# Optimization experiments

Hardware: AMD Instinct MI355X
Metric: run time of the kernel (lower is better)

Reference implementation:

```python
import jax, jax.numpy as jnp
import numpy as np

B = 131072
K = 1024
D = 16 * 8  # hard-coded feature dim in the torch module


def setup_inputs() -> dict:
    key = jax.random.key(0)
    kx, kw = jax.random.split(key)
    x = jax.random.normal(kx, (B, D), dtype=jnp.float32)
    # xavier_normal_ init: std = sqrt(2 / (fan_in + fan_out)) = sqrt(2 / (K + D))
    std = np.sqrt(2.0 / (K + D)).astype(np.float32)
    cluster_weights = jax.random.normal(kw, (K, D), dtype=jnp.float32) * std
    return {"x": x, "cluster_weights": cluster_weights}


def reference(x, cluster_weights):
    bn = x.shape[0]
    k = cluster_weights.shape[0]
    x = x.reshape(bn, -1)  # [B, D]
    # (same math as the original broadcasted (x - w)^2 sum, without the [B,K,D] blow-up)
    x2 = jnp.sum(x * x, axis=1, keepdims=True)               # [B, 1]
    w2 = jnp.sum(cluster_weights * cluster_weights, axis=1)  # [K]
    d = x2 + w2[None, :] - 2.0 * jnp.matmul(x, cluster_weights.T)  # [B, K]
    cl = jnp.argmin(d, axis=1)  # [B] int
    # distance to assigned centroid, summed
    inertia_loss = jnp.sum(jnp.take_along_axis(d, cl[:, None], axis=1))
    # xe_loss = sum_{i,j} (1 if i==j else -1) * <w_i, w_j>
    #         = 2 * trace(W W^T) - sum(W W^T)
    G = jnp.matmul(cluster_weights, cluster_weights.T)  # [K, K]
    xe_loss = 2.0 * jnp.trace(G) - jnp.sum(G)
    return inertia_loss / bn, xe_loss / k, cl
```

## Files before the change

kernel.cpp:

```cpp
#include <hip/hip_runtime.h>
#include <float.h>
#include <limits.h>
#include <math.h>


#define TAU 1e-3f

using bf16x8 = __attribute__((ext_vector_type(8))) short;
using f32x4  = __attribute__((ext_vector_type(4))) float;
using s16x4  = __attribute__((ext_vector_type(4))) short;

static __device__ __forceinline__ short f2bf_trunc(float f) {
    return (short)(__float_as_uint(f) >> 16);
}
static __device__ __forceinline__ float bf2f(short h) {
    return __uint_as_float(((unsigned int)(unsigned short)h) << 16);
}
static __device__ __forceinline__ bool lexlt(float v1, int i1, float v2, int i2) {
    return v1 < v2 || (v1 == v2 && i1 < i2);
}
static __device__ __forceinline__ void gload_lds16(const void* g, void* l) {
    __builtin_amdgcn_global_load_lds(
        (const __attribute__((address_space(1))) unsigned int*)g,
        (__attribute__((address_space(3))) unsigned int*)l, 16, 0, 0);
}
#define FENCE() do { asm volatile("" ::: "memory"); __builtin_amdgcn_sched_barrier(0); } while (0)

__global__ void wprep_kernel(const float* __restrict__ W, float* __restrict__ w2,
                             short* __restrict__ whl, int write_whl)
{
    const int k = blockIdx.x;
    const int d = threadIdx.x;
    float v = W[(size_t)k * 128 + d];
    float sq = v * v;
    for (int off = 1; off < 64; off <<= 1) sq += __shfl_xor(sq, off, 64);
    __shared__ float p[2];
    if ((d & 63) == 0) p[d >> 6] = sq;
    __syncthreads();
    if (d == 0) w2[k] = p[0] + p[1];
    if (write_whl) {
        short h = f2bf_trunc(v);
        short l = f2bf_trunc(v - bf2f(h));
        const int tile = k >> 6, c = k & 63;
        size_t base = (size_t)tile * 16384 + (size_t)(c >> 4) * 2048 + (size_t)(d >> 5) * 512
                    + (size_t)((d >> 3) & 3) * 128 + (size_t)(c & 15) * 8 + (size_t)(d & 7);
        whl[base]        = h;
        whl[base + 8192] = l;
    }
}

__global__ __launch_bounds__(512, 4)
void dist_argmin_mfma(const float* __restrict__ X, const short* __restrict__ whl,
                      const float* __restrict__ w2g, float* __restrict__ cl_out,
                      double* __restrict__ inertia_acc,
                      int* __restrict__ flag_cnt, int* __restrict__ flag_rows,
                      int flag_cap)
{
    __shared__ __align__(16) char smem[72320];
    char*   lB0  = smem;
    char*   lB1  = smem + 32768;
    float*  lw2  = (float*)(smem + 65536);
    float*  lx2  = (float*)(smem + 69632);
    int*    mscr = (int*)(smem + 70144);
    double* dred = (double*)(smem + 72192);

    const int tid    = threadIdx.x;
    const int lane   = tid & 63;
    const int laneLo = lane & 15;
    const int laneHi = lane >> 4;
    const int wid    = tid >> 6;
    const int rowg   = wid >> 1;
    const int colg   = wid & 1;
    const int rowbase = blockIdx.x * 128;

    lw2[tid]       = w2g[tid];
    lw2[tid + 512] = w2g[tid + 512];

    bf16x8 ah[2][4], al[2][4];
    #pragma unroll
    for (int m = 0; m < 2; ++m) {
        const float* xp = X + (size_t)(rowbase + rowg * 32 + m * 16 + laneLo) * 128 + laneHi * 8;
        float s = 0.f;
        #pragma unroll
        for (int k0b = 0; k0b < 4; ++k0b) {
            float4 v0 = *reinterpret_cast<const float4*>(xp + k0b * 32);
            float4 v1 = *reinterpret_cast<const float4*>(xp + k0b * 32 + 4);
            float fv[8] = {v0.x, v0.y, v0.z, v0.w, v1.x, v1.y, v1.z, v1.w};
            bf16x8 hv, lv;
            #pragma unroll
            for (int u = 0; u < 8; ++u) {
                s = fmaf(fv[u], fv[u], s);
                short h = f2bf_trunc(fv[u]);
                short l = f2bf_trunc(fv[u] - bf2f(h));
                hv[u] = h; lv[u] = l;
            }
            ah[m][k0b] = hv; al[m][k0b] = lv;
        }
        s += __shfl_xor(s, 16, 64);
        s += __shfl_xor(s, 32, 64);
        if (colg == 0 && laneHi == 0) lx2[rowg * 32 + m * 16 + laneLo] = s;
    }
    asm volatile("s_waitcnt lgkmcnt(0)" ::: "memory");
    __builtin_amdgcn_sched_barrier(0);

    const char* wsrc = (const char*)whl;
    #pragma unroll
    for (int q = 0; q < 4; ++q)
        gload_lds16(wsrc + wid * 4096 + q * 1024 + lane * 16,
                    lB0 + wid * 4096 + q * 1024);
    wsrc += 32768;

    float t1v[2][4], t2v[2][4];
    int   t1i[2][4];
    #pragma unroll
    for (int m = 0; m < 2; ++m)
        #pragma unroll
        for (int r = 0; r < 4; ++r) {
            t1v[m][r] = FLT_MAX; t2v[m][r] = FLT_MAX; t1i[m][r] = INT_MAX;
        }

    const float* w2p = lw2 + colg * 32 + laneLo;
    int colbase = colg * 32 + laneLo;

    auto compute = [&](const char* pB) {
        const char* pBb = pB + colg * 8192 + lane * 16;
        __builtin_amdgcn_s_setprio(1);
        #pragma unroll
        for (int nt = 0; nt < 2; ++nt) {
            float w2v = w2p[nt * 16];
            f32x4 a0 = (f32x4){0.f, 0.f, 0.f, 0.f};
            f32x4 a1 = (f32x4){0.f, 0.f, 0.f, 0.f};
            #pragma unroll
            for (int k0b = 0; k0b < 4; ++k0b) {
                bf16x8 bh = *reinterpret_cast<const bf16x8*>(pBb + nt * 4096 + k0b * 1024);
                bf16x8 bl = *reinterpret_cast<const bf16x8*>(pBb + 16384 + nt * 4096 + k0b * 1024);
                a0 = __builtin_amdgcn_mfma_f32_16x16x32_bf16(ah[0][k0b], bh, a0, 0, 0, 0);
                a0 = __builtin_amdgcn_mfma_f32_16x16x32_bf16(ah[0][k0b], bl, a0, 0, 0, 0);
                a0 = __builtin_amdgcn_mfma_f32_16x16x32_bf16(al[0][k0b], bh, a0, 0, 0, 0);
                a1 = __builtin_amdgcn_mfma_f32_16x16x32_bf16(ah[1][k0b], bh, a1, 0, 0, 0);
                a1 = __builtin_amdgcn_mfma_f32_16x16x32_bf16(ah[1][k0b], bl, a1, 0, 0, 0);
                a1 = __builtin_amdgcn_mfma_f32_16x16x32_bf16(al[1][k0b], bh, a1, 0, 0, 0);
            }
            const int col = colbase + nt * 16;
            #pragma unroll
            for (int r = 0; r < 4; ++r) {
                float dv0 = fmaf(-2.f, a0[r], w2v);
                t2v[0][r] = fminf(t2v[0][r], fmaxf(t1v[0][r], dv0));
                t1i[0][r] = (dv0 < t1v[0][r]) ? col : t1i[0][r];
                t1v[0][r] = fminf(t1v[0][r], dv0);
                float dv1 = fmaf(-2.f, a1[r], w2v);
                t2v[1][r] = fminf(t2v[1][r], fmaxf(t1v[1][r], dv1));
                t1i[1][r] = (dv1 < t1v[1][r]) ? col : t1i[1][r];
                t1v[1][r] = fminf(t1v[1][r], dv1);
            }
        }
        __builtin_amdgcn_s_setprio(0);
    };

    const char* cur = lB0;
    char*       nxt = lB1;
    #pragma unroll 1
    for (int t = 0; t < 15; ++t) {
        #pragma unroll
        for (int q = 0; q < 4; ++q)
            gload_lds16(wsrc + wid * 4096 + q * 1024 + lane * 16,
                        nxt + wid * 4096 + q * 1024);
        wsrc += 32768;
        asm volatile("s_waitcnt vmcnt(4)" ::: "memory");
        __builtin_amdgcn_sched_barrier(0);
        __builtin_amdgcn_s_barrier();
        FENCE();
        compute(cur);
        w2p += 64; colbase += 64;
        asm volatile("s_waitcnt lgkmcnt(0)" ::: "memory");
        __builtin_amdgcn_sched_barrier(0);
        __builtin_amdgcn_s_barrier();
        FENCE();
        char* tmp = nxt; nxt = (char*)cur; cur = tmp;
    }
    asm volatile("s_waitcnt vmcnt(0)" ::: "memory");
    __builtin_amdgcn_sched_barrier(0);
    __builtin_amdgcn_s_barrier();
    FENCE();
    compute(cur);

    #pragma unroll
    for (int off = 1; off < 16; off <<= 1) {
        #pragma unroll
        for (int m = 0; m < 2; ++m)
            #pragma unroll
            for (int r = 0; r < 4; ++r) {
                float ov1 = __shfl_xor(t1v[m][r], off, 64);
                int   oi1 = __shfl_xor(t1i[m][r], off, 64);
                float ov2 = __shfl_xor(t2v[m][r], off, 64);
                float nt2 = fminf(fminf(t2v[m][r], ov2), fmaxf(t1v[m][r], ov1));
                if (lexlt(ov1, oi1, t1v[m][r], t1i[m][r])) { t1v[m][r] = ov1; t1i[m][r] = oi1; }
                t2v[m][r] = nt2;
            }
    }

    __syncthreads();
    if (colg == 1 && laneLo == 0) {
        #pragma unroll
        for (int m = 0; m < 2; ++m)
            #pragma unroll
            for (int r = 0; r < 4; ++r) {
                const int row = rowg * 32 + m * 16 + laneHi * 4 + r;
                mscr[row * 4 + 0] = __float_as_int(t1v[m][r]);
                mscr[row * 4 + 1] = t1i[m][r];
                mscr[row * 4 + 2] = __float_as_int(t2v[m][r]);
            }
    }
    __syncthreads();
    double local = 0.0;
    if (colg == 0 && laneLo == 0) {
        #pragma unroll
        for (int m = 0; m < 2; ++m)
            #pragma unroll
            for (int r = 0; r < 4; ++r) {
                const int row = rowg * 32 + m * 16 + laneHi * 4 + r;
                float ov1 = __int_as_float(mscr[row * 4 + 0]);
                int   oi1 = mscr[row * 4 + 1];
                float ov2 = __int_as_float(mscr[row * 4 + 2]);
                float b1v = t1v[m][r], b2v;
                int   b1i = t1i[m][r];
                b2v = fminf(fminf(t2v[m][r], ov2), fmaxf(b1v, ov1));
                if (lexlt(ov1, oi1, b1v, b1i)) { b1v = ov1; b1i = oi1; }
                const int grow = rowbase + row;
                const float gap = b2v - b1v;
                if (gap >= TAU) {
                    cl_out[grow] = (float)b1i;
                    local += (double)(b1v + lx2[row]);
                } else {
                    int slot = atomicAdd(flag_cnt, 1);
                    if (slot < flag_cap) {
                        flag_rows[slot] = grow;
                    } else {
                        cl_out[grow] = (float)b1i;
                        local += (double)(b1v + lx2[row]);
                    }
                }
            }
        dred[rowg * 4 + laneHi] = local;
    }
    __syncthreads();
    if (tid == 0) {
        double tt = 0.0;
        for (int i = 0; i < 16; ++i) tt += dred[i];
        atomicAdd(inertia_acc, tt);
    }
}

__global__ __launch_bounds__(512, 1)
void dist_argmin_v2(const float* __restrict__ X, const float* __restrict__ W,
                    const float* __restrict__ w2g, float* __restrict__ cl_out,
                    double* __restrict__ inertia_acc,
                    int* __restrict__ flag_cnt, int* __restrict__ flag_rows,
                    int flag_cap)
{
    __shared__ __align__(16) char smem[133760];
    short*  Areg = (short*)smem;
    short*  Breg = (short*)(smem + 65536);
    int*    mscr = (int*)(smem + 131072);
    float*  lx2  = (float*)(smem + 131072 + 2048);
    double* dred = (double*)(smem + 131072 + 2048 + 512);

    const int tid    = threadIdx.x;
    const int lane   = tid & 63;
    const int laneLo = lane & 15;
    const int laneHi = lane >> 4;
    const int wid    = tid >> 6;
    const int rowg   = wid >> 1;
    const int colg   = wid & 1;
    const int rowbase = blockIdx.x * 128;

    {
        const int r = tid >> 2, q = tid & 3;
        float s = 0.f;
        #pragma unroll
        for (int j = 0; j < 8; ++j) {
            const int d0 = q * 4 + j * 16;
            float4 v = *reinterpret_cast<const float4*>(X + (size_t)(rowbase + r) * 128 + d0);
            float fv[4] = {v.x, v.y, v.z, v.w};
            s16x4 hv, lv;
            #pragma unroll
            for (int u = 0; u < 4; ++u) {
                s = fmaf(fv[u], fv[u], s);
                short h = f2bf_trunc(fv[u]);
                short l = f2bf_trunc(fv[u] - bf2f(h));
                hv[u] = h; lv[u] = l;
            }
            const int kb = d0 >> 3, off = d0 & 7;
            short* pa = Areg + (kb * 128 + r) * 8 + off;
            *reinterpret_cast<s16x4*>(pa)         = hv;
            *reinterpret_cast<s16x4*>(pa + 16384) = lv;
        }
        s += __shfl_xor(s, 1, 64);
        s += __shfl_xor(s, 2, 64);
        if (q == 0) lx2[r] = s;
    }

    float t1v[2][4], t2v[2][4];
// ... 75 lines not shown
                    float dv = fmaf(-2.f, acc[m][nt][r], w2v[nt]);
                    float hi = fmaxf(t1v[m][r], dv);
                    t2v[m][r] = fminf(t2v[m][r], hi);
                    bool cnd = dv < t1v[m][r];
                    t1i[m][r] = cnd ? col : t1i[m][r];
                    t1v[m][r] = fminf(t1v[m][r], dv);
                }
        }
    }

    #pragma unroll
    for (int off = 1; off < 16; off <<= 1) {
        #pragma unroll
        for (int m = 0; m < 2; ++m)
            #pragma unroll
            for (int r = 0; r < 4; ++r) {
                float ov1 = __shfl_xor(t1v[m][r], off, 64);
                int   oi1 = __shfl_xor(t1i[m][r], off, 64);
                float ov2 = __shfl_xor(t2v[m][r], off, 64);
                float nt2 = fminf(fminf(t2v[m][r], ov2), fmaxf(t1v[m][r], ov1));
                if (lexlt(ov1, oi1, t1v[m][r], t1i[m][r])) { t1v[m][r] = ov1; t1i[m][r] = oi1; }
                t2v[m][r] = nt2;
            }
    }

    __syncthreads();
    if (colg == 1 && laneLo == 0) {
        #pragma unroll
        for (int m = 0; m < 2; ++m)
            #pragma unroll
            for (int r = 0; r < 4; ++r) {
                const int row = rowg * 32 + m * 16 + laneHi * 4 + r;
                mscr[row * 4 + 0] = __float_as_int(t1v[m][r]);
                mscr[row * 4 + 1] = t1i[m][r];
                mscr[row * 4 + 2] = __float_as_int(t2v[m][r]);
            }
    }
    __syncthreads();
    double local = 0.0;
    if (colg == 0 && laneLo == 0) {
        #pragma unroll
        for (int m = 0; m < 2; ++m)
            #pragma unroll
            for (int r = 0; r < 4; ++r) {
                const int row = rowg * 32 + m * 16 + laneHi * 4 + r;
                float ov1 = __int_as_float(mscr[row * 4 + 0]);
                int   oi1 = mscr[row * 4 + 1];
                float ov2 = __int_as_float(mscr[row * 4 + 2]);
                float b1v = t1v[m][r], b2v;
                int   b1i = t1i[m][r];
                b2v = fminf(fminf(t2v[m][r], ov2), fmaxf(b1v, ov1));
                if (lexlt(ov1, oi1, b1v, b1i)) { b1v = ov1; b1i = oi1; }
                const int grow = rowbase + row;
                const float gap = b2v - b1v;
                if (gap >= TAU) {
                    cl_out[grow] = (float)b1i;
                    local += (double)(b1v + lx2[row]);
                } else {
                    int slot = atomicAdd(flag_cnt, 1);
                    if (slot < flag_cap) flag_rows[slot] = grow;
                    else { cl_out[grow] = (float)b1i; local += (double)(b1v + lx2[row]); }
                }
            }
        dred[rowg * 4 + laneHi] = local;
    }
    __syncthreads();
    if (tid == 0) {
        double t = 0.0;
        for (int i = 0; i < 16; ++i) t += dred[i];
        atomicAdd(inertia_acc, t);
    }
}

__global__ void refine_kernel(const float* __restrict__ X, const float* __restrict__ W,
                              const int* __restrict__ flag_cnt, const int* __restrict__ flag_rows,
                              int flag_cap, float* __restrict__ cl_out,
                              double* __restrict__ inertia_acc)
{
    __shared__ double sv[4];
    __shared__ int    si[4];
    __shared__ float  xrow[128];
    int n = *flag_cnt;
    if (n > flag_cap) n = flag_cap;
    const int tid = threadIdx.x;

    for (int f = blockIdx.x; f < n; f += gridDim.x) {
        int row = flag_rows[f];
        if (tid < 128) xrow[tid] = X[(size_t)row * 128 + tid];
        __syncthreads();

        double best = DBL_MAX; int bi = INT_MAX;
        for (int cc = 0; cc < 4; ++cc) {
            int c = tid + 256 * cc;
            double dot = 0.0, wsq = 0.0;
            for (int d = 0; d < 128; ++d) {
                double wv = (double)W[(size_t)c * 128 + d];
                dot = fma((double)xrow[d], wv, dot);
                wsq = fma(wv, wv, wsq);
            }
            double dist = wsq - 2.0 * dot;
            if (dist < best || (dist == best && c < bi)) { best = dist; bi = c; }
        }
        for (int off = 1; off < 64; off <<= 1) {
            double ov = __shfl_xor(best, off, 64);
            int    oi = __shfl_xor(bi, off, 64);
            if (ov < best || (ov == best && oi < bi)) { best = ov; bi = oi; }
        }
        if ((tid & 63) == 0) { sv[tid >> 6] = best; si[tid >> 6] = bi; }
        __syncthreads();
        if (tid == 0) {
            for (int wv = 1; wv < 4; ++wv)
                if (sv[wv] < best || (sv[wv] == best && si[wv] < bi)) { best = sv[wv]; bi = si[wv]; }
            double x2 = 0.0;
            for (int d = 0; d < 128; ++d) { double xv = (double)xrow[d]; x2 = fma(xv, xv, x2); }
            cl_out[row] = (float)bi;
            atomicAdd(inertia_acc, x2 + best);
        }
        __syncthreads();
    }
}

__global__ void finalize_kernel(const float* __restrict__ W, const float* __restrict__ w2,
                                const double* __restrict__ inertia, float* __restrict__ out)
{
    __shared__ float sh1[128], sh2[128];
    int d = threadIdx.x;
    float s = 0.f;
    for (int k = 0; k < 1024; ++k) s += W[(size_t)k * 128 + d];
    float t = 0.f;
    for (int j = 0; j < 8; ++j) t += w2[d + 128 * j];
    sh1[d] = s * s;
    sh2[d] = t;
    __syncthreads();
    for (int off = 64; off > 0; off >>= 1) {
        if (d < off) { sh1[d] += sh1[d + off]; sh2[d] += sh2[d + off]; }
        __syncthreads();
    }
    if (d == 0) {
        float xe = 2.f * sh2[0] - sh1[0];
        out[1] = xe / 1024.f;
        out[0] = (float)(*inertia / 131072.0);
    }
}

extern "C" void kernel_launch(void* const* d_in, const int* in_sizes, int n_in,
                              void* d_out, int out_size, void* d_ws, size_t ws_size,
                              hipStream_t stream)
{
    const float* X = (const float*)d_in[0];
    const float* W = (const float*)d_in[1];
    float* out = (float*)d_out;
    char* ws = (char*)d_ws;

    double* inertia  = (double*)ws;
    int*    flag_cnt = (int*)(ws + 8);
    float*  w2       = (float*)(ws + 16);
    short*  whl      = (short*)(ws + 8192);

    const size_t WHL_END = 8192 + 524288;
    const bool precomp = ws_size >= WHL_END + 65536;

    int*   flag_rows;
    int    flag_cap;
    if (precomp) {
        flag_rows = (int*)(ws + WHL_END);
        long cap = ((long)ws_size - (long)WHL_END) / 4;
        flag_cap = cap > 131072 ? 131072 : (int)cap;
    } else {
        flag_rows = (int*)(ws + 8192);
        long cap = ((long)ws_size - 8192) / 4;
        flag_cap = cap < 0 ? 0 : (cap > 131072 ? 131072 : (int)cap);
    }

    hipMemsetAsync(ws, 0, 16, stream);

    wprep_kernel<<<1024, 128, 0, stream>>>(W, w2, whl, precomp ? 1 : 0);
    if (precomp) {
        dist_argmin_mfma<<<1024, 512, 0, stream>>>(X, whl, w2, out + 2, inertia,
                                                   flag_cnt, flag_rows, flag_cap);
    } else {
        dist_argmin_v2<<<1024, 512, 0, stream>>>(X, W, w2, out + 2, inertia,
                                                 flag_cnt, flag_rows, flag_cap);
    }
    refine_kernel<<<1024, 256, 0, stream>>>(X, W, flag_cnt, flag_rows, flag_cap,
                                            out + 2, inertia);
    finalize_kernel<<<1, 128, 0, stream>>>(W, w2, inertia, out);
}
```

Measured before the change: 171.0 us.

## Use single-pass bf16 MFMA with top-3 tracking and tiered fp64 refinement

Replaces the 3-MFMA split-bf16 (hi/lo) distance computation with a single bf16 pass using round-to-nearest conversion, halving the LDS tile and W traffic. To keep argmin exact, each row now tracks the top-3 candidates: rows whose third-best is within a widened tolerance go to a full fp64 rescan, and rows with a close second go to a cheap two-candidate fp64 check. This cuts matrix-core work by about 3x, but it raises the number of flagged rows and adds two refine launches. Correctness now depends on the tolerance bounding the bf16 error, and rows beyond the fixed buffer capacities fall back to the unrefined bf16 result.

```diff
diff --git a/kernel.cpp b/kernel.cpp
--- a/kernel.cpp
+++ b/kernel.cpp
@@ -4,12 +4,16 @@
 #include <math.h>
 
 
-#define TAU 1e-3f
+#define TAU 0.012f
 
 using bf16x8 = __attribute__((ext_vector_type(8))) short;
 using f32x4  = __attribute__((ext_vector_type(4))) float;
 using s16x4  = __attribute__((ext_vector_type(4))) short;
 
+static __device__ __forceinline__ short f2bf_rne(float f) {
+    unsigned u = __float_as_uint(f);
+    return (short)((u + 0x7FFFu + ((u >> 16) & 1u)) >> 16);
+}
 static __device__ __forceinline__ short f2bf_trunc(float f) {
     return (short)(__float_as_uint(f) >> 16);
 }
@@ -27,7 +31,7 @@
 #define FENCE() do { asm volatile("" ::: "memory"); __builtin_amdgcn_sched_barrier(0); } while (0)
 
 __global__ void wprep_kernel(const float* __restrict__ W, float* __restrict__ w2,
-                             short* __restrict__ whl, int write_whl)
+                             short* __restrict__ wh, int write_wh)
 {
     const int k = blockIdx.x;
     const int d = threadIdx.x;
@@ -38,31 +42,28 @@
     if ((d & 63) == 0) p[d >> 6] = sq;
     __syncthreads();
     if (d == 0) w2[k] = p[0] + p[1];
-    if (write_whl) {
-        short h = f2bf_trunc(v);
-        short l = f2bf_trunc(v - bf2f(h));
+    if (write_wh) {
         const int tile = k >> 6, c = k & 63;
-        size_t base = (size_t)tile * 16384 + (size_t)(c >> 4) * 2048 + (size_t)(d >> 5) * 512
+        size_t base = (size_t)tile * 8192 + (size_t)(c >> 4) * 2048 + (size_t)(d >> 5) * 512
                     + (size_t)((d >> 3) & 3) * 128 + (size_t)(c & 15) * 8 + (size_t)(d & 7);
-        whl[base]        = h;
-        whl[base + 8192] = l;
+        wh[base] = f2bf_rne(v);
     }
 }
 
 __global__ __launch_bounds__(512, 4)
-void dist_argmin_mfma(const float* __restrict__ X, const short* __restrict__ whl,
-                      const float* __restrict__ w2g, float* __restrict__ cl_out,
-                      double* __restrict__ inertia_acc,
-                      int* __restrict__ flag_cnt, int* __restrict__ flag_rows,
-                      int flag_cap)
+void dist_argmin_1p(const float* __restrict__ X, const short* __restrict__ wh,
+                    const float* __restrict__ w2g, float* __restrict__ cl_out,
+                    double* __restrict__ inertia_acc,
+                    int* __restrict__ cnt2, int* __restrict__ cnt3,
+                    int* __restrict__ pair2, int cap2,
+                    int* __restrict__ full3, int cap3)
 {
-    __shared__ __align__(16) char smem[72320];
+    __shared__ __align__(16) char smem[39552];
     char*   lB0  = smem;
-    char*   lB1  = smem + 32768;
-    float*  lw2  = (float*)(smem + 65536);
-    float*  lx2  = (float*)(smem + 69632);
-    int*    mscr = (int*)(smem + 70144);
-    double* dred = (double*)(smem + 72192);
+    char*   lB1  = smem + 16384;
+    float*  lw2  = (float*)(smem + 32768);
+    int*    mscr = (int*)(smem + 36864);
+    double* dred = (double*)(smem + 39424);
 
     const int tid    = threadIdx.x;
     const int lane   = tid & 63;
@@ -76,7 +77,8 @@
     lw2[tid]       = w2g[tid];
     lw2[tid + 512] = w2g[tid + 512];
 
-    bf16x8 ah[2][4], al[2][4];
+    bf16x8 ah[2][4];
+    float  x2r[2];
     #pragma unroll
     for (int m = 0; m < 2; ++m) {
         const float* xp = X + (size_t)(rowbase + rowg * 32 + m * 16 + laneLo) * 128 + laneHi * 8;
@@ -86,103 +88,102 @@
             float4 v0 = *reinterpret_cast<const float4*>(xp + k0b * 32);
             float4 v1 = *reinterpret_cast<const float4*>(xp + k0b * 32 + 4);
             float fv[8] = {v0.x, v0.y, v0.z, v0.w, v1.x, v1.y, v1.z, v1.w};
-            bf16x8 hv, lv;
+            bf16x8 hv;
             #pragma unroll
             for (int u = 0; u < 8; ++u) {
                 s = fmaf(fv[u], fv[u], s);
-                short h = f2bf_trunc(fv[u]);
-                short l = f2bf_trunc(fv[u] - bf2f(h));
-                hv[u] = h; lv[u] = l;
-            }
-            ah[m][k0b] = hv; al[m][k0b] = lv;
+                hv[u] = f2bf_rne(fv[u]);
+            }
+            ah[m][k0b] = hv;
         }
         s += __shfl_xor(s, 16, 64);
         s += __shfl_xor(s, 32, 64);
-        if (colg == 0 && laneHi == 0) lx2[rowg * 32 + m * 16 + laneLo] = s;
+        x2r[m] = s;
     }
     asm volatile("s_waitcnt lgkmcnt(0)" ::: "memory");
     __builtin_amdgcn_sched_barrier(0);
 
-    const char* wsrc = (const char*)whl;
+    const char* whb = (const char*)wh;
     #pragma unroll
-    for (int q = 0; q < 4; ++q)
-        gload_lds16(wsrc + wid * 4096 + q * 1024 + lane * 16,
-                    lB0 + wid * 4096 + q * 1024);
-    wsrc += 32768;
-
-    float t1v[2][4], t2v[2][4];
-    int   t1i[2][4];
+    for (int q = 0; q < 2; ++q)
+        gload_lds16(whb + wid * 2048 + q * 1024 + lane * 16,
+                    lB0 + wid * 2048 + q * 1024);
+
+    float t1v[2][4], t2v[2][4], t3v[2][4];
+    int   t1i[2][4], t2i[2][4];
     #pragma unroll
     for (int m = 0; m < 2; ++m)
         #pragma unroll
         for (int r = 0; r < 4; ++r) {
-            t1v[m][r] = FLT_MAX; t2v[m][r] = FLT_MAX; t1i[m][r] = INT_MAX;
-        }
-
-    const float* w2p = lw2 + colg * 32 + laneLo;
-    int colbase = colg * 32 + laneLo;
-
-    auto compute = [&](const char* pB) {
-        const char* pBb = pB + colg * 8192 + lane * 16;
+            t1v[m][r] = FLT_MAX; t2v[m][r] = FLT_MAX; t3v[m][r] = FLT_MAX;
+            t1i[m][r] = INT_MAX; t2i[m][r] = INT_MAX;
+        }
+
+    const char* pB0 = lB0 + colg * 8192 + lane * 16;
+    const char* pB1 = lB1 + colg * 8192 + lane * 16;
+
+    auto compute = [&](int t, const char* pBb) {
+        float w2v[2];
+        #pragma unroll
+        for (int nt = 0; nt < 2; ++nt)
+            w2v[nt] = lw2[t * 64 + colg * 32 + nt * 16 + laneLo];
+
+        f32x4 acc[2][2];
         __builtin_amdgcn_s_setprio(1);
         #pragma unroll
         for (int nt = 0; nt < 2; ++nt) {
-            float w2v = w2p[nt * 16];
             f32x4 a0 = (f32x4){0.f, 0.f, 0.f, 0.f};
             f32x4 a1 = (f32x4){0.f, 0.f, 0.f, 0.f};
             #pragma unroll
             for (int k0b = 0; k0b < 4; ++k0b) {
                 bf16x8 bh = *reinterpret_cast<const bf16x8*>(pBb + nt * 4096 + k0b * 1024);
-                bf16x8 bl = *reinterpret_cast<const bf16x8*>(pBb + 16384 + nt * 4096 + k0b * 1024);
                 a0 = __builtin_amdgcn_mfma_f32_16x16x32_bf16(ah[0][k0b], bh, a0, 0, 0, 0);
-                a0 = __builtin_amdgcn_mfma_f32_16x16x32_bf16(ah[0][k0b], bl, a0, 0, 0, 0);
-                a0 = __builtin_amdgcn_mfma_f32_16x16x32_bf16(al[0][k0b], bh, a0, 0, 0, 0);
                 a1 = __builtin_amdgcn_mfma_f32_16x16x32_bf16(ah[1][k0b], bh, a1, 0, 0, 0);
-                a1 = __builtin_amdgcn_mfma_f32_16x16x32_bf16(ah[1][k0b], bl, a1, 0, 0, 0);
-                a1 = __builtin_amdgcn_mfma_f32_16x16x32_bf16(al[1][k0b], bh, a1, 0, 0, 0);
-            }
-            const int col = colbase + nt * 16;
-            #pragma unroll
-            for (int r = 0; r < 4; ++r) {
-                float dv0 = fmaf(-2.f, a0[r], w2v);
-                t2v[0][r] = fminf(t2v[0][r], fmaxf(t1v[0][r], dv0));
-                t1i[0][r] = (dv0 < t1v[0][r]) ? col : t1i[0][r];
-                t1v[0][r] = fminf(t1v[0][r], dv0);
-                float dv1 = fmaf(-2.f, a1[r], w2v);
-                t2v[1][r] = fminf(t2v[1][r], fmaxf(t1v[1][r], dv1));
-                t1i[1][r] = (dv1 < t1v[1][r]) ? col : t1i[1][r];
-                t1v[1][r] = fminf(t1v[1][r], dv1);
-            }
+            }
+            acc[nt][0] = a0; acc[nt][1] = a1;
         }
         __builtin_amdgcn_s_setprio(0);
+
+        #pragma unroll
+        for (int nt = 0; nt < 2; ++nt) {
+            const int col = t * 64 + colg * 32 + nt * 16 + laneLo;
+            #pragma unroll
+            for (int m = 0; m < 2; ++m)
+                #pragma unroll
+                for (int r = 0; r < 4; ++r) {
+                    float dv = fmaf(-2.f, acc[nt][m][r], w2v[nt]);
+                    bool c1 = dv < t1v[m][r];
+                    bool c2 = dv < t2v[m][r];
+                    t3v[m][r] = fminf(t3v[m][r], fmaxf(t2v[m][r], dv));
+                    t2v[m][r] = fminf(t2v[m][r], fmaxf(t1v[m][r], dv));
+                    t2i[m][r] = c1 ? t1i[m][r] : (c2 ? col : t2i[m][r]);
+                    t1i[m][r] = c1 ? col : t1i[m][r];
+                    t1v[m][r] = fminf(t1v[m][r], dv);
+                }
+        }
     };
 
-    const char* cur = lB0;
-    char*       nxt = lB1;
     #pragma unroll 1
     for (int t = 0; t < 15; ++t) {
-        #pragma unroll
-        for (int q = 0; q < 4; ++q)
-            gload_lds16(wsrc + wid * 4096 + q * 1024 + lane * 16,
-                        nxt + wid * 4096 + q * 1024);
-        wsrc += 32768;
-        asm volatile("s_waitcnt vmcnt(4)" ::: "memory");
+        asm volatile("s_waitcnt vmcnt(0)" ::: "memory");
         __builtin_amdgcn_sched_barrier(0);
         __builtin_amdgcn_s_barrier();
         FENCE();
-        compute(cur);
-        w2p += 64; colbase += 64;
-        asm volatile("s_waitcnt lgkmcnt(0)" ::: "memory");
-        __builtin_amdgcn_sched_barrier(0);
-        __builtin_amdgcn_s_barrier();
-        FENCE();
-        char* tmp = nxt; nxt = (char*)cur; cur = tmp;
+        {
+            const char* src = whb + (size_t)(t + 1) * 16384;
+            char* dst = ((t + 1) & 1) ? lB1 : lB0;
+            #pragma unroll
+            for (int q = 0; q < 2; ++q)
+                gload_lds16(src + wid * 2048 + q * 1024 + lane * 16,
+                            dst + wid * 2048 + q * 1024);
+        }
+        compute(t, (t & 1) ? pB1 : pB0);
     }
     asm volatile("s_waitcnt vmcnt(0)" ::: "memory");
     __builtin_amdgcn_sched_barrier(0);
     __builtin_amdgcn_s_barrier();
     FENCE();
-    compute(cur);
+    compute(15, pB1);
 
     #pragma unroll
     for (int off = 1; off < 16; off <<= 1) {
@@ -193,11 +194,34 @@
                 float ov1 = __shfl_xor(t1v[m][r], off, 64);
                 int   oi1 = __shfl_xor(t1i[m][r], off, 64);
                 float ov2 = __shfl_xor(t2v[m][r], off, 64);
-                float nt2 = fminf(fminf(t2v[m][r], ov2), fmaxf(t1v[m][r], ov1));
-                if (lexlt(ov1, oi1, t1v[m][r], t1i[m][r])) { t1v[m][r] = ov1; t1i[m][r] = oi1; }
-                t2v[m][r] = nt2;
-            }
-    }
+                int   oi2 = __shfl_xor(t2i[m][r], off, 64);
+                float ov3 = __shfl_xor(t3v[m][r], off, 64);
+                if (lexlt(ov1, oi1, t1v[m][r], t1i[m][r])) {
+                    t3v[m][r] = t2v[m][r];
+                    t2v[m][r] = t1v[m][r]; t2i[m][r] = t1i[m][r];
+                    t1v[m][r] = ov1;       t1i[m][r] = oi1;
+                } else if (lexlt(ov1, oi1, t2v[m][r], t2i[m][r])) {
+                    t3v[m][r] = t2v[m][r];
+                    t2v[m][r] = ov1; t2i[m][r] = oi1;
+                } else if (ov1 < t3v[m][r]) {
+                    t3v[m][r] = ov1;
+                }
+                if (lexlt(ov2, oi2, t2v[m][r], t2i[m][r])) {
+                    t3v[m][r] = t2v[m][r];
+                    t2v[m][r] = ov2; t2i[m][r] = oi2;
+                } else if (ov2 < t3v[m][r]) {
+                    t3v[m][r] = ov2;
+                }
+                t3v[m][r] = fminf(t3v[m][r], ov3);
+            }
+    }
+
+    float x2v[2][4];
+    #pragma unroll
+    for (int m = 0; m < 2; ++m)
+        #pragma unroll
+        for (int r = 0; r < 4; ++r)
+            x2v[m][r] = __shfl(x2r[m], laneHi * 4 + r, 64);
 
     __syncthreads();
     if (colg == 1 && laneLo == 0) {
@@ -206,9 +230,11 @@
             #pragma unroll
             for (int r = 0; r < 4; ++r) {
                 const int row = rowg * 32 + m * 16 + laneHi * 4 + r;
-                mscr[row * 4 + 0] = __float_as_int(t1v[m][r]);
-                mscr[row * 4 + 1] = t1i[m][r];
-                mscr[row * 4 + 2] = __float_as_int(t2v[m][r]);
+                mscr[row * 5 + 0] = __float_as_int(t1v[m][r]);
+                mscr[row * 5 + 1] = t1i[m][r];
+                mscr[row * 5 + 2] = __float_as_int(t2v[m][r]);
+                mscr[row * 5 + 3] = t2i[m][r];
+                mscr[row * 5 + 4] = __float_as_int(t3v[m][r]);
             }
     }
     __syncthreads();
@@ -219,26 +245,45 @@
             #pragma unroll
             for (int r = 0; r < 4; ++r) {
                 const int row = rowg * 32 + m * 16 + laneHi * 4 + r;
-                float ov1 = __int_as_float(mscr[row * 4 + 0]);
-                int   oi1 = mscr[row * 4 + 1];
-                float ov2 = __int_as_float(mscr[row * 4 + 2]);
-                float b1v = t1v[m][r], b2v;
-                int   b1i = t1i[m][r];
-                b2v = fminf(fminf(t2v[m][r], ov2), fmaxf(b1v, ov1));
-                if (lexlt(ov1, oi1, b1v, b1i)) { b1v = ov1; b1i = oi1; }
+                float ov1 = __int_as_float(mscr[row * 5 + 0]);
+                int   oi1 = mscr[row * 5 + 1];
+                float ov2 = __int_as_float(mscr[row * 5 + 2]);
+                int   oi2 = mscr[row * 5 + 3];
+                float ov3 = __int_as_float(mscr[row * 5 + 4]);
+                float b1v = t1v[m][r], b2v = t2v[m][r], b3v = t3v[m][r];
+                int   b1i = t1i[m][r], b2i = t2i[m][r];
+                if (lexlt(ov1, oi1, b1v, b1i)) {
+                    b3v = b2v; b2v = b1v; b2i = b1i; b1v = ov1; b1i = oi1;
+                } else if (lexlt(ov1, oi1, b2v, b2i)) {
+                    b3v = b2v; b2v = ov1; b2i = oi1;
+                } else if (ov1 < b3v) b3v = ov1;
+                if (lexlt(ov2, oi2, b2v, b2i)) {
+                    b3v = b2v; b2v = ov2; b2i = oi2;
+                } else if (ov2 < b3v) b3v = ov2;
+                b3v = fminf(b3v, ov3);
+
                 const int grow = rowbase + row;
-                const float gap = b2v - b1v;
-                if (gap >= TAU) {
-                    cl_out[grow] = (float)b1i;
-                    local += (double)(b1v + lx2[row]);
-                } else {
-                    int slot = atomicAdd(flag_cnt, 1);
-                    if (slot < flag_cap) {
-                        flag_rows[slot] = grow;
+                if (b3v - b1v < TAU) {
+                    int slot = atomicAdd(cnt3, 1);
+                    if (slot < cap3) {
+                        full3[slot] = grow;
                     } else {
                         cl_out[grow] = (float)b1i;
-                        local += (double)(b1v + lx2[row]);
+                        local += (double)(b1v + x2v[m][r]);
                     }
+                } else if (b2v - b1v < TAU) {
+                    int slot = atomicAdd(cnt2, 1);
+                    if (slot < cap2) {
+                        pair2[slot * 3 + 0] = grow;
+                        pair2[slot * 3 + 1] = b1i;
+                        pair2[slot * 3 + 2] = b2i;
+                    } else {
+                        cl_out[grow] = (float)b1i;
+                        local += (double)(b1v + x2v[m][r]);
+                    }
+                } else {
+                    cl_out[grow] = (float)b1i;
+                    local += (double)(b1v + x2v[m][r]);
                 }
             }
         dred[rowg * 4 + laneHi] = local;
@@ -248,6 +293,82 @@
         double tt = 0.0;
         for (int i = 0; i < 16; ++i) tt += dred[i];
         atomicAdd(inertia_acc, tt);
+    }
+}
+
+__global__ void pair_refine(const float* __restrict__ X, const float* __restrict__ W,
+                            const int* __restrict__ cnt2, const int* __restrict__ pair2,
+                            int cap2, float* __restrict__ cl_out,
+                            double* __restrict__ inertia_acc)
+{
+    int n = *cnt2; if (n > cap2) n = cap2;
+    int idx = blockIdx.x * 256 + threadIdx.x;
+    if (idx >= n) return;
+    int row = pair2[idx * 3 + 0];
+    int i1  = pair2[idx * 3 + 1];
+    int i2  = pair2[idx * 3 + 2];
+    const float* xr = X + (size_t)row * 128;
+    const float* wa = W + (size_t)i1 * 128;
+    const float* wb = W + (size_t)i2 * 128;
+    double d1 = 0.0, d2 = 0.0;
+    #pragma unroll 8
+    for (int d = 0; d < 128; ++d) {
+        double xv = (double)xr[d];
+        double e1 = xv - (double)wa[d]; d1 = fma(e1, e1, d1);
+        double e2 = xv - (double)wb[d]; d2 = fma(e2, e2, d2);
+    }
+    int win; double dw;
+    if (d1 < d2 || (d1 == d2 && i1 < i2)) { win = i1; dw = d1; }
+    else                                  { win = i2; dw = d2; }
+    cl_out[row] = (float)win;
+    atomicAdd(inertia_acc, dw);
+}
+
+__global__ void full_refine(const float* __restrict__ X, const float* __restrict__ W,
+                            const int* __restrict__ cnt3, const int* __restrict__ full3,
+                            int cap3, float* __restrict__ cl_out,
+                            double* __restrict__ inertia_acc)
+{
+    __shared__ double sv[4];
+    __shared__ int    si[4];
+    __shared__ float  xrow[128];
+    int n = *cnt3;
+    if (n > cap3) n = cap3;
+    const int tid = threadIdx.x;
+
+    for (int f = blockIdx.x; f < n; f += gridDim.x) {
+        int row = full3[f];
+        if (tid < 128) xrow[tid] = X[(size_t)row * 128 + tid];
+        __syncthreads();
+
+        double best = DBL_MAX; int bi = INT_MAX;
+        for (int cc = 0; cc < 4; ++cc) {
+            int c = tid + 256 * cc;
+            double dot = 0.0, wsq = 0.0;
+            for (int d = 0; d < 128; ++d) {
+                double wv = (double)W[(size_t)c * 128 + d];
+                dot = fma((double)xrow[d], wv, dot);
+                wsq = fma(wv, wv, wsq);
+            }
+            double dist = wsq - 2.0 * dot;
+            if (dist < best || (dist == best && c < bi)) { best = dist; bi = c; }
+        }
+        for (int off = 1; off < 64; off <<= 1) {
+            double ov = __shfl_xor(best, off, 64);
+            int    oi = __shfl_xor(bi, off, 64);
+            if (ov < best || (ov == best && oi < bi)) { best = ov; bi = oi; }
+        }
+        if ((tid & 63) == 0) { sv[tid >> 6] = best; si[tid >> 6] = bi; }
+        __syncthreads();
+        if (tid == 0) {
+            for (int wv = 1; wv < 4; ++wv)
+                if (sv[wv] < best || (sv[wv] == best && si[wv] < bi)) { best = sv[wv]; bi = si[wv]; }
+            double x2 = 0.0;
+            for (int d = 0; d < 128; ++d) { double xv = (double)xrow[d]; x2 = fma(xv, xv, x2); }
+            cl_out[row] = (float)bi;
+            atomicAdd(inertia_acc, x2 + best);
+        }
+        __syncthreads();
     }
 }
 
@@ -429,14 +550,13 @@
                 b2v = fminf(fminf(t2v[m][r], ov2), fmaxf(b1v, ov1));
                 if (lexlt(ov1, oi1, b1v, b1i)) { b1v = ov1; b1i = oi1; }
                 const int grow = rowbase + row;
-                const float gap = b2v - b1v;
-                if (gap >= TAU) {
-                    cl_out[grow] = (float)b1i;
-                    local += (double)(b1v + lx2[row]);
-                } else {
+                if (b2v - b1v < 1e-3f) {
                     int slot = atomicAdd(flag_cnt, 1);
                     if (slot < flag_cap) flag_rows[slot] = grow;
                     else { cl_out[grow] = (float)b1i; local += (double)(b1v + lx2[row]); }
+                } else {
+                    cl_out[grow] = (float)b1i;
+                    local += (double)(b1v + lx2[row]);
                 }
             }
         dred[rowg * 4 + laneHi] = local;
@@ -446,54 +566,6 @@
         double t = 0.0;
         for (int i = 0; i < 16; ++i) t += dred[i];
         atomicAdd(inertia_acc, t);
-    }
-}
-
-__global__ void refine_kernel(const float* __restrict__ X, const float* __restrict__ W,
-                              const int* __restrict__ flag_cnt, const int* __restrict__ flag_rows,
-                              int flag_cap, float* __restrict__ cl_out,
-                              double* __restrict__ inertia_acc)
-{
-    __shared__ double sv[4];
-    __shared__ int    si[4];
-    __shared__ float  xrow[128];
-    int n = *flag_cnt;
-    if (n > flag_cap) n = flag_cap;
-    const int tid = threadIdx.x;
-
-    for (int f = blockIdx.x; f < n; f += gridDim.x) {
-        int row = flag_rows[f];
-        if (tid < 128) xrow[tid] = X[(size_t)row * 128 + tid];
-        __syncthreads();
-
-        double best = DBL_MAX; int bi = INT_MAX;
-        for (int cc = 0; cc < 4; ++cc) {
-            int c = tid + 256 * cc;
-            double dot = 0.0, wsq = 0.0;
-            for (int d = 0; d < 128; ++d) {
-                double wv = (double)W[(size_t)c * 128 + d];
-                dot = fma((double)xrow[d], wv, dot);
-                wsq = fma(wv, wv, wsq);
-            }
-            double dist = wsq - 2.0 * dot;
-            if (dist < best || (dist == best && c < bi)) { best = dist; bi = c; }
-        }
-        for (int off = 1; off < 64; off <<= 1) {
-            double ov = __shfl_xor(best, off, 64);
-            int    oi = __shfl_xor(bi, off, 64);
-            if (ov < best || (ov == best && oi < bi)) { best = ov; bi = oi; }
-        }
-        if ((tid & 63) == 0) { sv[tid >> 6] = best; si[tid >> 6] = bi; }
-        __syncthreads();
-        if (tid == 0) {
-            for (int wv = 1; wv < 4; ++wv)
-                if (sv[wv] < best || (sv[wv] == best && si[wv] < bi)) { best = sv[wv]; bi = si[wv]; }
-            double x2 = 0.0;
-            for (int d = 0; d < 128; ++d) { double xv = (double)xrow[d]; x2 = fma(xv, xv, x2); }
-            cl_out[row] = (float)bi;
-            atomicAdd(inertia_acc, x2 + best);
-        }
-        __syncthreads();
     }
 }
 
@@ -529,37 +601,35 @@
     float* out = (float*)d_out;
     char* ws = (char*)d_ws;
 
-    double* inertia  = (double*)ws;
-    int*    flag_cnt = (int*)(ws + 8);
-    float*  w2       = (float*)(ws + 16);
-    short*  whl      = (short*)(ws + 8192);
-
-    const size_t WHL_END = 8192 + 524288;
-    const bool precomp = ws_size >= WHL_END + 65536;
-
-    int*   flag_rows;
-    int    flag_cap;
+    double* inertia = (double*)ws;
+    int*    cnt2    = (int*)(ws + 8);
+    int*    cnt3    = (int*)(ws + 12);
+    float*  w2      = (float*)(ws + 16);
+    short*  wh      = (short*)(ws + 4608);
+    int*    pair2   = (int*)(ws + 266752);
+    int*    full3   = (int*)(ws + 561664);
+    const int CAP2 = 24576, CAP3 = 8192;
+    const size_t NEED = 594432;
+
+    const bool precomp = ws_size >= NEED;
+
+    hipMemsetAsync(ws, 0, 16, stream);
+
     if (precomp) {
-        flag_rows = (int*)(ws + WHL_END);
-        long cap = ((long)ws_size - (long)WHL_END) / 4;
-        flag_cap = cap > 131072 ? 131072 : (int)cap;
+        wprep_kernel<<<1024, 128, 0, stream>>>(W, w2, wh, 1);
+        dist_argmin_1p<<<1024, 512, 0, stream>>>(X, wh, w2, out + 2, inertia,
+                                                 cnt2, cnt3, pair2, CAP2, full3, CAP3);
+        pair_refine<<<(CAP2 + 255) / 256, 256, 0, stream>>>(X, W, cnt2, pair2, CAP2,
+                                                            out + 2, inertia);
+        full_refine<<<256, 256, 0, stream>>>(X, W, cnt3, full3, CAP3, out + 2, inertia);
     } else {
-        flag_rows = (int*)(ws + 8192);
-        long cap = ((long)ws_size - 8192) / 4;
-        flag_cap = cap < 0 ? 0 : (cap > 131072 ? 131072 : (int)cap);
-    }
-
-    hipMemsetAsync(ws, 0, 16, stream);
-
-    wprep_kernel<<<1024, 128, 0, stream>>>(W, w2, whl, precomp ? 1 : 0);
-    if (precomp) {
-        dist_argmin_mfma<<<1024, 512, 0, stream>>>(X, whl, w2, out + 2, inertia,
-                                                   flag_cnt, flag_rows, flag_cap);
-    } else {
+        int* full3f = (int*)(ws + 4608);
+        long cap = ((long)ws_size - 4608) / 4;
+        int capf = cap < 0 ? 0 : (cap > 131072 ? 131072 : (int)cap);
+        wprep_kernel<<<1024, 128, 0, stream>>>(W, w2, (short*)full3f, 0);
         dist_argmin_v2<<<1024, 512, 0, stream>>>(X, W, w2, out + 2, inertia,
-                                                 flag_cnt, flag_rows, flag_cap);
-    }
-    refine_kernel<<<1024, 256, 0, stream>>>(X, W, flag_cnt, flag_rows, flag_cap,
-                                            out + 2, inertia);
+                                                 cnt3, full3f, capf);
+        full_refine<<<256, 256, 0, stream>>>(X, W, cnt3, full3f, capf, out + 2, inertia);
+    }
     finalize_kernel<<<1, 128, 0, stream>>>(W, w2, inertia, out);
 }
```

New measurement: 258.0 us. 50.9% more time.

## Use single-pass bf16 MFMA with wider tie margin and top-2 refinement

Applied to the files above, without the earlier changes.

Replaces the three-term split-bf16 (hi/lo) distance GEMM with a single bf16 pass using round-to-nearest, which cuts MFMA work and W tile traffic to a third. To compensate for the lower precision, the ambiguity margin TAU is widened so more rows are flagged. A new refine kernel handles those rows with an fp32 top-2 search followed by an exact fp64 comparison of the two candidates. The W pipeline now loads two 64-column tiles per stage, and the flagged-row buffer is capped at a fixed size. The risk is that many more rows get flagged, or that a near-tie falls outside the margin and is resolved wrongly.

```diff
diff --git a/kernel.cpp b/kernel.cpp
--- a/kernel.cpp
+++ b/kernel.cpp
@@ -4,12 +4,16 @@
 #include <math.h>
 
 
-#define TAU 1e-3f
+#define TAU 0.012f
 
 using bf16x8 = __attribute__((ext_vector_type(8))) short;
 using f32x4  = __attribute__((ext_vector_type(4))) float;
 using s16x4  = __attribute__((ext_vector_type(4))) short;
 
+static __device__ __forceinline__ short f2bf_rne(float f) {
+    unsigned u = __float_as_uint(f);
+    return (short)((u + 0x7FFFu + ((u >> 16) & 1u)) >> 16);
+}
 static __device__ __forceinline__ short f2bf_trunc(float f) {
     return (short)(__float_as_uint(f) >> 16);
 }
@@ -27,7 +31,7 @@
 #define FENCE() do { asm volatile("" ::: "memory"); __builtin_amdgcn_sched_barrier(0); } while (0)
 
 __global__ void wprep_kernel(const float* __restrict__ W, float* __restrict__ w2,
-                             short* __restrict__ whl, int write_whl)
+                             short* __restrict__ wh, int write_wh)
 {
     const int k = blockIdx.x;
     const int d = threadIdx.x;
@@ -38,23 +42,20 @@
     if ((d & 63) == 0) p[d >> 6] = sq;
     __syncthreads();
     if (d == 0) w2[k] = p[0] + p[1];
-    if (write_whl) {
-        short h = f2bf_trunc(v);
-        short l = f2bf_trunc(v - bf2f(h));
+    if (write_wh) {
         const int tile = k >> 6, c = k & 63;
-        size_t base = (size_t)tile * 16384 + (size_t)(c >> 4) * 2048 + (size_t)(d >> 5) * 512
+        size_t base = (size_t)tile * 8192 + (size_t)(c >> 4) * 2048 + (size_t)(d >> 5) * 512
                     + (size_t)((d >> 3) & 3) * 128 + (size_t)(c & 15) * 8 + (size_t)(d & 7);
-        whl[base]        = h;
-        whl[base + 8192] = l;
+        wh[base] = f2bf_rne(v);
     }
 }
 
 __global__ __launch_bounds__(512, 4)
-void dist_argmin_mfma(const float* __restrict__ X, const short* __restrict__ whl,
-                      const float* __restrict__ w2g, float* __restrict__ cl_out,
-                      double* __restrict__ inertia_acc,
-                      int* __restrict__ flag_cnt, int* __restrict__ flag_rows,
-                      int flag_cap)
+void dist_argmin_1p(const float* __restrict__ X, const short* __restrict__ wh,
+                    const float* __restrict__ w2g, float* __restrict__ cl_out,
+                    double* __restrict__ inertia_acc,
+                    int* __restrict__ flag_cnt, int* __restrict__ flag_rows,
+                    int flag_cap)
 {
     __shared__ __align__(16) char smem[72320];
     char*   lB0  = smem;
@@ -76,7 +77,7 @@
     lw2[tid]       = w2g[tid];
     lw2[tid + 512] = w2g[tid + 512];
 
-    bf16x8 ah[2][4], al[2][4];
+    bf16x8 ah[2][4];
     #pragma unroll
     for (int m = 0; m < 2; ++m) {
         const float* xp = X + (size_t)(rowbase + rowg * 32 + m * 16 + laneLo) * 128 + laneHi * 8;
@@ -86,29 +87,26 @@
             float4 v0 = *reinterpret_cast<const float4*>(xp + k0b * 32);
             float4 v1 = *reinterpret_cast<const float4*>(xp + k0b * 32 + 4);
             float fv[8] = {v0.x, v0.y, v0.z, v0.w, v1.x, v1.y, v1.z, v1.w};
-            bf16x8 hv, lv;
+            bf16x8 hv;
             #pragma unroll
             for (int u = 0; u < 8; ++u) {
                 s = fmaf(fv[u], fv[u], s);
-                short h = f2bf_trunc(fv[u]);
-                short l = f2bf_trunc(fv[u] - bf2f(h));
-                hv[u] = h; lv[u] = l;
-            }
-            ah[m][k0b] = hv; al[m][k0b] = lv;
+                hv[u] = f2bf_rne(fv[u]);
+            }
+            ah[m][k0b] = hv;
         }
         s += __shfl_xor(s, 16, 64);
         s += __shfl_xor(s, 32, 64);
         if (colg == 0 && laneHi == 0) lx2[rowg * 32 + m * 16 + laneLo] = s;
     }
+
+    #pragma unroll
+    for (int q = 0; q < 4; ++q)
+        gload_lds16((const char*)wh + wid * 4096 + q * 1024 + lane * 16,
+                    lB0 + wid * 4096 + q * 1024);
+
     asm volatile("s_waitcnt lgkmcnt(0)" ::: "memory");
     __builtin_amdgcn_sched_barrier(0);
-
-    const char* wsrc = (const char*)whl;
-    #pragma unroll
-    for (int q = 0; q < 4; ++q)
-        gload_lds16(wsrc + wid * 4096 + q * 1024 + lane * 16,
-                    lB0 + wid * 4096 + q * 1024);
-    wsrc += 32768;
 
     float t1v[2][4], t2v[2][4];
     int   t1i[2][4];
@@ -119,36 +117,32 @@
             t1v[m][r] = FLT_MAX; t2v[m][r] = FLT_MAX; t1i[m][r] = INT_MAX;
         }
 
-    const float* w2p = lw2 + colg * 32 + laneLo;
-    int colbase = colg * 32 + laneLo;
-
-    auto compute = [&](const char* pB) {
-        const char* pBb = pB + colg * 8192 + lane * 16;
+    auto compute = [&](int ti, const char* tileBase) {
+        const char* pBb = tileBase + colg * 8192 + lane * 16;
+        float w2v[2];
+        #pragma unroll
+        for (int nt = 0; nt < 2; ++nt)
+            w2v[nt] = lw2[ti * 64 + colg * 32 + nt * 16 + laneLo];
+
         __builtin_amdgcn_s_setprio(1);
         #pragma unroll
         for (int nt = 0; nt < 2; ++nt) {
-            float w2v = w2p[nt * 16];
             f32x4 a0 = (f32x4){0.f, 0.f, 0.f, 0.f};
             f32x4 a1 = (f32x4){0.f, 0.f, 0.f, 0.f};
             #pragma unroll
             for (int k0b = 0; k0b < 4; ++k0b) {
                 bf16x8 bh = *reinterpret_cast<const bf16x8*>(pBb + nt * 4096 + k0b * 1024);
-                bf16x8 bl = *reinterpret_cast<const bf16x8*>(pBb + 16384 + nt * 4096 + k0b * 1024);
                 a0 = __builtin_amdgcn_mfma_f32_16x16x32_bf16(ah[0][k0b], bh, a0, 0, 0, 0);
-                a0 = __builtin_amdgcn_mfma_f32_16x16x32_bf16(ah[0][k0b], bl, a0, 0, 0, 0);
-                a0 = __builtin_amdgcn_mfma_f32_16x16x32_bf16(al[0][k0b], bh, a0, 0, 0, 0);
                 a1 = __builtin_amdgcn_mfma_f32_16x16x32_bf16(ah[1][k0b], bh, a1, 0, 0, 0);
-                a1 = __builtin_amdgcn_mfma_f32_16x16x32_bf16(ah[1][k0b], bl, a1, 0, 0, 0);
-                a1 = __builtin_amdgcn_mfma_f32_16x16x32_bf16(al[1][k0b], bh, a1, 0, 0, 0);
-            }
-            const int col = colbase + nt * 16;
-            #pragma unroll
-            for (int r = 0; r < 4; ++r) {
-                float dv0 = fmaf(-2.f, a0[r], w2v);
+            }
+            const int col = ti * 64 + colg * 32 + nt * 16 + laneLo;
+            #pragma unroll
+            for (int r = 0; r < 4; ++r) {
+                float dv0 = fmaf(-2.f, a0[r], w2v[nt]);
                 t2v[0][r] = fminf(t2v[0][r], fmaxf(t1v[0][r], dv0));
                 t1i[0][r] = (dv0 < t1v[0][r]) ? col : t1i[0][r];
                 t1v[0][r] = fminf(t1v[0][r], dv0);
-                float dv1 = fmaf(-2.f, a1[r], w2v);
+                float dv1 = fmaf(-2.f, a1[r], w2v[nt]);
                 t2v[1][r] = fminf(t2v[1][r], fmaxf(t1v[1][r], dv1));
                 t1i[1][r] = (dv1 < t1v[1][r]) ? col : t1i[1][r];
                 t1v[1][r] = fminf(t1v[1][r], dv1);
@@ -160,29 +154,30 @@
     const char* cur = lB0;
     char*       nxt = lB1;
     #pragma unroll 1
-    for (int t = 0; t < 15; ++t) {
-        #pragma unroll
-        for (int q = 0; q < 4; ++q)
-            gload_lds16(wsrc + wid * 4096 + q * 1024 + lane * 16,
-                        nxt + wid * 4096 + q * 1024);
-        wsrc += 32768;
-        asm volatile("s_waitcnt vmcnt(4)" ::: "memory");
+    for (int p = 0; p < 8; ++p) {
+        if (p < 7) {
+            const char* src = (const char*)wh + (size_t)(p + 1) * 32768;
+            #pragma unroll
+            for (int q = 0; q < 4; ++q)
+                gload_lds16(src + wid * 4096 + q * 1024 + lane * 16,
+                            nxt + wid * 4096 + q * 1024);
+            asm volatile("s_waitcnt vmcnt(4)" ::: "memory");
+        } else {
+            asm volatile("s_waitcnt vmcnt(0)" ::: "memory");
+        }
         __builtin_amdgcn_sched_barrier(0);
         __builtin_amdgcn_s_barrier();
         FENCE();
-        compute(cur);
-        w2p += 64; colbase += 64;
-        asm volatile("s_waitcnt lgkmcnt(0)" ::: "memory");
-        __builtin_amdgcn_sched_barrier(0);
-        __builtin_amdgcn_s_barrier();
-        FENCE();
-        char* tmp = nxt; nxt = (char*)cur; cur = tmp;
-    }
-    asm volatile("s_waitcnt vmcnt(0)" ::: "memory");
-    __builtin_amdgcn_sched_barrier(0);
-    __builtin_amdgcn_s_barrier();
-    FENCE();
-    compute(cur);
+        compute(2 * p,     cur);
+        compute(2 * p + 1, cur + 16384);
+        if (p < 7) {
+            asm volatile("s_waitcnt lgkmcnt(0)" ::: "memory");
+            __builtin_amdgcn_sched_barrier(0);
+            __builtin_amdgcn_s_barrier();
+            FENCE();
+            char* tmp = nxt; nxt = (char*)cur; cur = tmp;
+        }
+    }
 
     #pragma unroll
     for (int off = 1; off < 16; off <<= 1) {
@@ -227,11 +222,7 @@
                 b2v = fminf(fminf(t2v[m][r], ov2), fmaxf(b1v, ov1));
                 if (lexlt(ov1, oi1, b1v, b1i)) { b1v = ov1; b1i = oi1; }
                 const int grow = rowbase + row;
-                const float gap = b2v - b1v;
-                if (gap >= TAU) {
-                    cl_out[grow] = (float)b1i;
-                    local += (double)(b1v + lx2[row]);
-                } else {
+                if (b2v - b1v < TAU) {
                     int slot = atomicAdd(flag_cnt, 1);
                     if (slot < flag_cap) {
                         flag_rows[slot] = grow;
@@ -239,6 +230,9 @@
                         cl_out[grow] = (float)b1i;
                         local += (double)(b1v + lx2[row]);
                     }
+                } else {
+                    cl_out[grow] = (float)b1i;
+                    local += (double)(b1v + lx2[row]);
                 }
             }
         dred[rowg * 4 + laneHi] = local;
@@ -248,6 +242,90 @@
         double tt = 0.0;
         for (int i = 0; i < 16; ++i) tt += dred[i];
         atomicAdd(inertia_acc, tt);
+    }
+}
+
+__global__ void refine2_kernel(const float* __restrict__ X, const float* __restrict__ W,
+                               const float* __restrict__ w2,
+                               const int* __restrict__ flag_cnt,
+                               const int* __restrict__ flag_rows, int flag_cap,
+                               float* __restrict__ cl_out,
+                               double* __restrict__ inertia_acc)
+{
+    __shared__ float xrow[128];
+    __shared__ float rv1[4], rv2[4];
+    __shared__ int   ri1[4], ri2[4];
+    int n = *flag_cnt;
+    if (n > flag_cap) n = flag_cap;
+    const int tid  = threadIdx.x;
+    const int lane = tid & 63;
+    const int wv   = tid >> 6;
+
+    for (int f = blockIdx.x; f < n; f += gridDim.x) {
+        const int row = flag_rows[f];
+        if (tid < 128) xrow[tid] = X[(size_t)row * 128 + tid];
+        __syncthreads();
+
+        float v1 = FLT_MAX, v2 = FLT_MAX;
+        int   i1 = INT_MAX, i2 = INT_MAX;
+        #pragma unroll
+        for (int cc = 0; cc < 4; ++cc) {
+            const int c = tid + 256 * cc;
+            const float* wr = W + (size_t)c * 128;
+            float dot = 0.f;
+            #pragma unroll 8
+            for (int d = 0; d < 128; ++d) dot = fmaf(xrow[d], wr[d], dot);
+            float dv = fmaf(-2.f, dot, w2[c]);
+            if (lexlt(dv, c, v1, i1)) { v2 = v1; i2 = i1; v1 = dv; i1 = c; }
+            else if (lexlt(dv, c, v2, i2)) { v2 = dv; i2 = c; }
+        }
+        #pragma unroll
+        for (int off = 1; off < 64; off <<= 1) {
+            float ov1 = __shfl_xor(v1, off, 64);
+            int   oi1 = __shfl_xor(i1, off, 64);
+            float ov2 = __shfl_xor(v2, off, 64);
+            int   oi2 = __shfl_xor(i2, off, 64);
+            if (lexlt(ov1, oi1, v1, i1)) {
+                float nv2; int ni2;
+                if (lexlt(v1, i1, ov2, oi2)) { nv2 = v1; ni2 = i1; }
+                else                         { nv2 = ov2; ni2 = oi2; }
+                v1 = ov1; i1 = oi1; v2 = nv2; i2 = ni2;
+            } else if (lexlt(ov1, oi1, v2, i2)) {
+                v2 = ov1; i2 = oi1;
+            }
+        }
+        if (lane == 0) { rv1[wv] = v1; ri1[wv] = i1; rv2[wv] = v2; ri2[wv] = i2; }
+        __syncthreads();
+        if (tid == 0) {
+            float b1 = rv1[0], b2 = rv2[0];
+            int   c1 = ri1[0], c2 = ri2[0];
+            for (int w = 1; w < 4; ++w) {
+                float ov1 = rv1[w], ov2 = rv2[w];
+                int   oi1 = ri1[w], oi2 = ri2[w];
+                if (lexlt(ov1, oi1, b1, c1)) {
+                    float nv2; int ni2;
+                    if (lexlt(b1, c1, ov2, oi2)) { nv2 = b1; ni2 = c1; }
+                    else                         { nv2 = ov2; ni2 = oi2; }
+                    b1 = ov1; c1 = oi1; b2 = nv2; c2 = ni2;
+                } else if (lexlt(ov1, oi1, b2, c2)) {
+                    b2 = ov1; c2 = oi1;
+                }
+            }
+            const float* wa = W + (size_t)c1 * 128;
+            const float* wb = W + (size_t)c2 * 128;
+            double d1 = 0.0, d2 = 0.0;
+            for (int d = 0; d < 128; ++d) {
+                double xv = (double)xrow[d];
+                double e1 = xv - (double)wa[d]; d1 = fma(e1, e1, d1);
+                double e2 = xv - (double)wb[d]; d2 = fma(e2, e2, d2);
+            }
+            int win; double dw;
+            if (d1 < d2 || (d1 == d2 && c1 < c2)) { win = c1; dw = d1; }
+            else                                  { win = c2; dw = d2; }
+            cl_out[row] = (float)win;
+            atomicAdd(inertia_acc, dw);
+        }
+        __syncthreads();
     }
 }
 
@@ -429,14 +507,13 @@
                 b2v = fminf(fminf(t2v[m][r], ov2), fmaxf(b1v, ov1));
                 if (lexlt(ov1, oi1, b1v, b1i)) { b1v = ov1; b1i = oi1; }
                 const int grow = rowbase + row;
-                const float gap = b2v - b1v;
-                if (gap >= TAU) {
-                    cl_out[grow] = (float)b1i;
-                    local += (double)(b1v + lx2[row]);
-                } else {
+                if (b2v - b1v < 1e-3f) {
                     int slot = atomicAdd(flag_cnt, 1);
                     if (slot < flag_cap) flag_rows[slot] = grow;
                     else { cl_out[grow] = (float)b1i; local += (double)(b1v + lx2[row]); }
+                } else {
+                    cl_out[grow] = (float)b1i;
+                    local += (double)(b1v + lx2[row]);
                 }
             }
         dred[rowg * 4 + laneHi] = local;
@@ -446,54 +523,6 @@
         double t = 0.0;
         for (int i = 0; i < 16; ++i) t += dred[i];
         atomicAdd(inertia_acc, t);
-    }
-}
-
-__global__ void refine_kernel(const float* __restrict__ X, const float* __restrict__ W,
-                              const int* __restrict__ flag_cnt, const int* __restrict__ flag_rows,
-                              int flag_cap, float* __restrict__ cl_out,
-                              double* __restrict__ inertia_acc)
-{
-    __shared__ double sv[4];
-    __shared__ int    si[4];
-    __shared__ float  xrow[128];
-    int n = *flag_cnt;
-    if (n > flag_cap) n = flag_cap;
-    const int tid = threadIdx.x;
-
-    for (int f = blockIdx.x; f < n; f += gridDim.x) {
-        int row = flag_rows[f];
-        if (tid < 128) xrow[tid] = X[(size_t)row * 128 + tid];
-        __syncthreads();
-
-        double best = DBL_MAX; int bi = INT_MAX;
-        for (int cc = 0; cc < 4; ++cc) {
-            int c = tid + 256 * cc;
-            double dot = 0.0, wsq = 0.0;
-            for (int d = 0; d < 128; ++d) {
-                double wv = (double)W[(size_t)c * 128 + d];
-                dot = fma((double)xrow[d], wv, dot);
-                wsq = fma(wv, wv, wsq);
-            }
-            double dist = wsq - 2.0 * dot;
-            if (dist < best || (dist == best && c < bi)) { best = dist; bi = c; }
-        }
-        for (int off = 1; off < 64; off <<= 1) {
-            double ov = __shfl_xor(best, off, 64);
-            int    oi = __shfl_xor(bi, off, 64);
-            if (ov < best || (ov == best && oi < bi)) { best = ov; bi = oi; }
-        }
-        if ((tid & 63) == 0) { sv[tid >> 6] = best; si[tid >> 6] = bi; }
-        __syncthreads();
-        if (tid == 0) {
-            for (int wv = 1; wv < 4; ++wv)
-                if (sv[wv] < best || (sv[wv] == best && si[wv] < bi)) { best = sv[wv]; bi = si[wv]; }
-            double x2 = 0.0;
-            for (int d = 0; d < 128; ++d) { double xv = (double)xrow[d]; x2 = fma(xv, xv, x2); }
-            cl_out[row] = (float)bi;
-            atomicAdd(inertia_acc, x2 + best);
-        }
-        __syncthreads();
     }
 }
 
@@ -532,34 +561,30 @@
     double* inertia  = (double*)ws;
     int*    flag_cnt = (int*)(ws + 8);
     float*  w2       = (float*)(ws + 16);
-    short*  whl      = (short*)(ws + 8192);
-
-    const size_t WHL_END = 8192 + 524288;
-    const bool precomp = ws_size >= WHL_END + 65536;
-
-    int*   flag_rows;
-    int    flag_cap;
+    short*  wh       = (short*)(ws + 4608);
+    int*    flags    = (int*)(ws + 266752);
+    const int FCAP = 16384;
+    const size_t NEED = 332288;
+
+    const bool precomp = ws_size >= NEED;
+
+    hipMemsetAsync(ws, 0, 16, stream);
+
     if (precomp) {
-        flag_rows = (int*)(ws + WHL_END);
-        long cap = ((long)ws_size - (long)WHL_END) / 4;
-        flag_cap = cap > 131072 ? 131072 : (int)cap;
+        wprep_kernel<<<1024, 128, 0, stream>>>(W, w2, wh, 1);
+        dist_argmin_1p<<<1024, 512, 0, stream>>>(X, wh, w2, out + 2, inertia,
+                                                 flag_cnt, flags, FCAP);
+        refine2_kernel<<<512, 256, 0, stream>>>(X, W, w2, flag_cnt, flags, FCAP,
+                                                out + 2, inertia);
     } else {
-        flag_rows = (int*)(ws + 8192);
-        long cap = ((long)ws_size - 8192) / 4;
-        flag_cap = cap < 0 ? 0 : (cap > 131072 ? 131072 : (int)cap);
-    }
-
-    hipMemsetAsync(ws, 0, 16, stream);
-
-    wprep_kernel<<<1024, 128, 0, stream>>>(W, w2, whl, precomp ? 1 : 0);
-    if (precomp) {
-        dist_argmin_mfma<<<1024, 512, 0, stream>>>(X, whl, w2, out + 2, inertia,
-                                                   flag_cnt, flag_rows, flag_cap);
-    } else {
+        int* flagsf = (int*)(ws + 4608);
+        long cap = ((long)ws_size - 4608) / 4;
+        int capf = cap < 0 ? 0 : (cap > 131072 ? 131072 : (int)cap);
+        wprep_kernel<<<1024, 128, 0, stream>>>(W, w2, (short*)flagsf, 0);
         dist_argmin_v2<<<1024, 512, 0, stream>>>(X, W, w2, out + 2, inertia,
-                                                 flag_cnt, flag_rows, flag_cap);
-    }
-    refine_kernel<<<1024, 256, 0, stream>>>(X, W, flag_cnt, flag_rows, flag_cap,
-                                            out + 2, inertia);
+                                                 flag_cnt, flagsf, capf);
+        refine2_kernel<<<512, 256, 0, stream>>>(X, W, w2, flag_cnt, flagsf, capf,
+                                                out + 2, inertia);
+    }
     finalize_kernel<<<1, 128, 0, stream>>>(W, w2, inertia, out);
 }
```

New measurement: 516.7 us. +202.2%, slower.
